# Performance work log

Hardware: AMD Instinct MI355X
Metric: run time of the kernel (lower is better)

## Reference

```python
import jax, jax.numpy as jnp
import numpy as np

NUM_GROUPS = 32
EPS = 1e-6


def group_norm(x, gamma, beta):
    # x: (B, C, H, W)
    B, C, H, W = x.shape
    g = x.reshape(B, NUM_GROUPS, C // NUM_GROUPS, H, W)
    mean = g.mean(axis=(2, 3, 4), keepdims=True)
    var = g.var(axis=(2, 3, 4), keepdims=True)
    g = (g - mean) / jnp.sqrt(var + EPS)
    g = g.reshape(B, C, H, W)
    return g * gamma[None, :, None, None] + beta[None, :, None, None]


def nin(x, W, b):
    # 1x1 linear projection over channel dim
    return jnp.einsum('bchw,cd->bdhw', x, W) + b[None, :, None, None]


def setup_inputs() -> dict:
    key = jax.random.key(0)
    ks = jax.random.split(key, 8)
    B, C, H, W = 32, 512, 32, 32
    lim = np.sqrt(3 * 0.1 / C)  # NIN init_scale=0.1 uniform limit
    return {
        'x': jax.random.normal(ks[0], (B, C, H, W), jnp.float32),
        'gamma': jnp.ones((C,), jnp.float32),
        'beta': jnp.zeros((C,), jnp.float32),
        'Wq': jax.random.uniform(ks[1], (C, C), jnp.float32, -lim, lim),
        'bq': jnp.zeros((C,), jnp.float32),
        'Wk': jax.random.uniform(ks[2], (C, C), jnp.float32, -lim, lim),
        'bk': jnp.zeros((C,), jnp.float32),
        'Wv': jax.random.uniform(ks[3], (C, C), jnp.float32, -lim, lim),
        'bv': jnp.zeros((C,), jnp.float32),
        'Wp': jax.random.normal(ks[4], (C, C), jnp.float32) * 1e-5,  # init_scale=0.0 -> ~0
        'bp': jnp.zeros((C,), jnp.float32),
    }


def reference(x, gamma, beta, Wq, bq, Wk, bk, Wv, bv, Wp, bp):
    B, C, H, W = x.shape
    h = group_norm(x, gamma, beta)
    q = nin(h, Wq, bq)
    k = nin(h, Wk, bk)
    v = nin(h, Wv, bv)
    # full (HW)x(HW) attention weights, as the original materializes
    w = jnp.einsum('bchw,bcHW->bhwHW', q, k) * (C ** -0.5)
    w = w.reshape(B, H, W, H * W)
    w = jax.nn.softmax(w, axis=-1)
    w = w.reshape(B, H, W, H, W)
    h_out = jnp.einsum('bhwHW,bcHW->bchw', w, v)
    h_out = nin(h_out, Wp, bp)
    return x + h_out
```

## Files before the change

### kernel.cpp

```cpp
#include <hip/hip_runtime.h>
#include <hip/hip_bf16.h>
#include <math.h>

typedef __attribute__((ext_vector_type(8))) short bf16x8;
typedef __attribute__((ext_vector_type(4))) float f32x4;

typedef const __attribute__((address_space(1))) unsigned int guint;
typedef __attribute__((address_space(3))) unsigned int luint;

static __device__ __forceinline__ short f2bf(float f) {
    union { float f; unsigned u; } a; a.f = f;
    unsigned r = 0x7FFFu + ((a.u >> 16) & 1u);
    return (short)((a.u + r) >> 16);
}
static __device__ __forceinline__ float bf2f(short s) {
    union { unsigned u; float f; } a;
    a.u = ((unsigned)(unsigned short)s) << 16;
    return a.f;
}

__global__ __launch_bounds__(256)
void prep_w(const float* __restrict__ Wq, const float* __restrict__ Wk,
            const float* __restrict__ Wp, const float* __restrict__ Wv,
            const float* __restrict__ bq, const float* __restrict__ bk,
            const float* __restrict__ bp, const float* __restrict__ bv,
            short* __restrict__ wT, float* __restrict__ bqk,
            float* __restrict__ b2, float qscale)
{
    const int z = blockIdx.z;
    const int t = threadIdx.x;
    if (z == 4) {
        if (blockIdx.y == 0 && blockIdx.x < 16) {
            __shared__ float red[256];
            const int o = blockIdx.x * 32 + (t >> 3);
            const int part = t & 7;
            float a = 0.f;
            for (int d = part * 64; d < part * 64 + 64; ++d)
                a += bv[d] * Wp[d * 512 + o];
            red[t] = a; __syncthreads();
            if (part < 4) red[t] += red[t + 4];
            __syncthreads();
            if (part < 2) red[t] += red[t + 2];
            __syncthreads();
            if (part == 0) b2[o] = red[t] + red[t + 1] + bp[o];
        } else if (blockIdx.y == 1 && blockIdx.x < 4) {
            int i = blockIdx.x * 256 + t;
            bqk[i] = (i < 512) ? bq[i] * qscale : bk[i - 512];
        }
        return;
    }
    const int tx = t & 31, ty = t >> 5;
    const int c0 = blockIdx.y * 32, d0 = blockIdx.x * 32;
    short* O = wT + (long long)z * 262144;
    if (z == 3) {
#pragma unroll
        for (int r = 0; r < 4; ++r) {
            const int idx = (c0 + ty + 8 * r) * 512 + d0 + tx;
            O[idx] = f2bf(Wv[idx]);
        }
        return;
    }
    __shared__ float ld[32][33];
    const float* W = (z == 0) ? Wq : (z == 1) ? Wk : Wp;
    const float sc = (z == 0) ? qscale : 1.f;
#pragma unroll
    for (int r = 0; r < 4; ++r)
        ld[ty + 8 * r][tx] = W[(long long)(c0 + ty + 8 * r) * 512 + d0 + tx];
    __syncthreads();
#pragma unroll
    for (int r = 0; r < 4; ++r)
        O[(long long)(d0 + ty + 8 * r) * 512 + c0 + tx] = f2bf(ld[tx][ty + 8 * r] * sc);
}

__global__ __launch_bounds__(256)
void small_nt(const short* __restrict__ A, const short* __restrict__ B,
              short* __restrict__ C, float scale, int K,
              int lda, int ldb, int ldc, int tilesM)
{
    __shared__ short lsA[128 * 64];
    __shared__ short lsB[128 * 64];
    const int m0 = (blockIdx.x % tilesM) * 128;
    const int n0 = (blockIdx.x / tilesM) * 128;
    const int t = threadIdx.x;
    const int lane = t & 63;
    const int w = t >> 6;
    const int wr = w >> 1, wc = w & 1;
    const int lr16 = lane & 15, lkg = lane >> 4;
    const int srow = 32 * w + (lane >> 3);
    const int scol = (lane & 7) * 8;
    const short* gA = A + (long long)(m0 + srow) * lda + scol;
    const short* gB = B + (long long)(n0 + srow) * ldb + scol;

    f32x4 acc[4][4];
#pragma unroll
    for (int i = 0; i < 4; ++i)
#pragma unroll
        for (int j = 0; j < 4; ++j) acc[i][j] = (f32x4){0.f, 0.f, 0.f, 0.f};

    const int nk = K >> 6;
    for (int kt = 0; kt < nk; ++kt) {
        const short* ga = gA + kt * 64;
        const short* gb = gB + kt * 64;
#pragma unroll
        for (int c = 0; c < 4; ++c) {
            __builtin_amdgcn_global_load_lds(
                (guint*)(ga + (long long)(8 * c) * lda),
                (luint*)&lsA[(32 * w + 8 * c) * 64], 16, 0, 0);
            __builtin_amdgcn_global_load_lds(
                (guint*)(gb + (long long)(8 * c) * ldb),
                (luint*)&lsB[(32 * w + 8 * c) * 64], 16, 0, 0);
        }
        __syncthreads();
#pragma unroll
        for (int ks = 0; ks < 2; ++ks) {
            bf16x8 af[4], bfr[4];
#pragma unroll
            for (int mi = 0; mi < 4; ++mi)
                af[mi] = *reinterpret_cast<const bf16x8*>(
                    &lsA[(wr * 64 + mi * 16 + lr16) * 64 + ks * 32 + lkg * 8]);
#pragma unroll
            for (int ni = 0; ni < 4; ++ni)
                bfr[ni] = *reinterpret_cast<const bf16x8*>(
                    &lsB[(wc * 64 + ni * 16 + lr16) * 64 + ks * 32 + lkg * 8]);
#pragma unroll
            for (int mi = 0; mi < 4; ++mi)
#pragma unroll
                for (int ni = 0; ni < 4; ++ni)
                    acc[mi][ni] = __builtin_amdgcn_mfma_f32_16x16x32_bf16(
                        af[mi], bfr[ni], acc[mi][ni], 0, 0, 0);
        }
        __syncthreads();
    }
#pragma unroll
    for (int mi = 0; mi < 4; ++mi)
#pragma unroll
        for (int ni = 0; ni < 4; ++ni) {
            const int col = n0 + wc * 64 + ni * 16 + lr16;
#pragma unroll
            for (int j = 0; j < 4; ++j) {
                const int rrow = m0 + wr * 64 + mi * 16 + lkg * 4 + j;
                C[(long long)rrow * ldc + col] = f2bf(acc[mi][ni][j] * scale);
            }
        }
}

__global__ __launch_bounds__(256)
void gn_fused(const float* __restrict__ x, const float* __restrict__ gamma,
              const float* __restrict__ beta, short* __restrict__ hn,
              short* __restrict__ hnT)
{
    __shared__ float xs[16 * 1024];
    __shared__ float red[256];
    const int bg = blockIdx.x;
    const int g  = bg & 31, b = bg >> 5;
    const int t  = threadIdx.x;
    const float4* px = reinterpret_cast<const float4*>(x + (long long)bg * 16384);
    float s = 0.f, ss = 0.f;
#pragma unroll
    for (int i = 0; i < 16; ++i) {
        float4 v = px[t + 256 * i];
        reinterpret_cast<float4*>(xs)[t + 256 * i] = v;
        s  += v.x + v.y + v.z + v.w;
        ss += v.x * v.x + v.y * v.y + v.z * v.z + v.w * v.w;
    }
    red[t] = s; __syncthreads();
    for (int o = 128; o > 0; o >>= 1) {
        if (t < o) red[t] += red[t + o];
        __syncthreads();
    }
    const float mean = red[0] * (1.f / 16384.f);
    __syncthreads();
    red[t] = ss; __syncthreads();
    for (int o = 128; o > 0; o >>= 1) {
        if (t < o) red[t] += red[t + o];
        __syncthreads();
    }
    const float var  = red[0] * (1.f / 16384.f) - mean * mean;
    const float rstd = rsqrtf(var + 1e-6f);

    const int half = t & 1;
    float ga[8], be[8];
#pragma unroll
    for (int cc = 0; cc < 8; ++cc) {
        ga[cc] = gamma[g * 16 + half * 8 + cc];
        be[cc] = beta[g * 16 + half * 8 + cc];
    }
    short* outB = hn + (long long)bg * 16384;
#pragma unroll
    for (int it = 0; it < 8; ++it) {
        const int sidx = it * 128 + (t >> 1);
        bf16x8 o;
#pragma unroll
        for (int cc = 0; cc < 8; ++cc) {
            float v = xs[(half * 8 + cc) * 1024 + sidx];
            o[cc] = f2bf((v - mean) * rstd * ga[cc] + be[cc]);
        }
        *reinterpret_cast<bf16x8*>(outB + sidx * 16 + half * 8) = o;
    }
    short* oT = hnT + ((long long)b * 512 + g * 16) * 1024;
#pragma unroll
    for (int cc = 0; cc < 16; ++cc) {
        const float g_ = gamma[g * 16 + cc], b_ = beta[g * 16 + cc];
        const int pos = t * 4;
        short4 o4;
        o4.x = f2bf((xs[cc * 1024 + pos + 0] - mean) * rstd * g_ + b_);
        o4.y = f2bf((xs[cc * 1024 + pos + 1] - mean) * rstd * g_ + b_);
        o4.z = f2bf((xs[cc * 1024 + pos + 2] - mean) * rstd * g_ + b_);
        o4.w = f2bf((xs[cc * 1024 + pos + 3] - mean) * rstd * g_ + b_);
        *reinterpret_cast<short4*>(oT + cc * 1024 + pos) = o4;
    }
}

template<int BIAS_M, int BIAS_N, int RESID, int EXPRS, int DIVROW4, int HN_A, int HN_B>
__global__ __launch_bounds__(512, 1)
void nt_gemm(const short* __restrict__ A, const short* __restrict__ B,
             void* __restrict__ Cv,
             const float* __restrict__ biasM, const float* __restrict__ biasN,
             const float* __restrict__ resid, float* __restrict__ rs,
             float scale, int K, int lda, int ldb, int ldc,
             long long sA, long long sB, long long sC,
             int tilesM, int tilesPerBatch)
{
    __shared__ short lsA[2][2][128 * 64];
    __shared__ short lsB[2][2][128 * 64];

    const int id = blockIdx.x;
    const int chunk = gridDim.x >> 3;
    const int gid = chunk ? ((id & 7) * chunk + (id >> 3)) : id;
    const int bz = gid / tilesPerBatch;
    const int tt = gid - bz * tilesPerBatch;
    const int m0 = (tt % tilesM) * 256;
    const int n0 = (tt / tilesM) * 256;

    const int t = threadIdx.x;
    const int lane = t & 63;
    const int w = t >> 6;
    const int wrs = w >> 1;
    const int wcs = w & 1;
    const int lr16 = lane & 15, lkg = lane >> 4;
    const int sw = lr16 & 7;

    const int srow = t >> 3;
    const int jch  = (t & 7) ^ (srow & 7);
    const int scol = jch * 8;

    const short* gA; int rsA, ktA;
    if (HN_A) {
        gA = A + ((long long)bz * 32 + (jch >> 1)) * 16384
               + (long long)(m0 + srow) * 16 + (jch & 1) * 8;
        rsA = 16; ktA = 65536;
    } else {
        gA = A + (long long)bz * sA + (long long)(m0 + srow) * lda + scol;
        rsA = lda; ktA = 64;
    }
    const short* gB; int rsB, ktB;
    if (HN_B) {
        gB = B + ((long long)bz * 32 + (jch >> 1)) * 16384
               + (long long)(n0 + srow) * 16 + (jch & 1) * 8;
        rsB = 16; ktB = 65536;
    } else {
        gB = B + (long long)bz * sB + (long long)(n0 + srow) * ldb + scol;
        rsB = ldb; ktB = 64;
    }

    f32x4 acc[4][2][4];
#pragma unroll
    for (int q = 0; q < 4; ++q)
#pragma unroll
        for (int i = 0; i < 2; ++i)
#pragma unroll
            for (int j = 0; j < 4; ++j) acc[q][i][j] = (f32x4){0.f, 0.f, 0.f, 0.f};

    const int nk = K >> 6;

#define STAGE_A(buf, h, kt)                                                    \
    {                                                                          \
        _Pragma("unroll")                                                      \
        for (int c = 0; c < 2; ++c)                                            \
            __builtin_amdgcn_global_load_lds(                                  \
                (guint*)(gA + (long long)(kt) * ktA                            \
                            + (long long)((h) * 128 + 64 * c) * rsA),          \
                (luint*)&lsA[buf][h][t * 8 + 4096 * c], 16, 0, 0);             \
    }
#define STAGE_B(buf, h, kt)                                                    \
    {                                                                          \
        _Pragma("unroll")                                                      \
        for (int c = 0; c < 2; ++c)                                            \
            __builtin_amdgcn_global_load_lds(                                  \
                (guint*)(gB + (long long)(kt) * ktB                            \
                            + (long long)((h) * 128 + 64 * c) * rsB),          \
                (luint*)&lsB[buf][h][t * 8 + 4096 * c], 16, 0, 0);             \
    }

#define LDA_HALF(dst, buf, h)                                                  \
    _Pragma("unroll")                                                          \
    for (int mi2 = 0; mi2 < 2; ++mi2)                                          \
        _Pragma("unroll")                                                      \
        for (int ks = 0; ks < 2; ++ks)                                         \
            dst[mi2][ks] = *reinterpret_cast<const bf16x8*>(                   \
                &lsA[buf][h][(wrs * 32 + mi2 * 16 + lr16) * 64 +               \
                             (((ks * 4 + lkg) ^ sw) * 8)]);
#define LDB_HALF(dst, buf, h)                                                  \
    _Pragma("unroll")                                                          \
    for (int ni = 0; ni < 4; ++ni)                                             \
        _Pragma("unroll")                                                      \
        for (int ks = 0; ks < 2; ++ks)                                         \
            dst[ni][ks] = *reinterpret_cast<const bf16x8*>(                    \
                &lsB[buf][h][(wcs * 64 + ni * 16 + lr16) * 64 +                \
                             (((ks * 4 + lkg) ^ sw) * 8)]);

#define MFMAQ(q, Af, Bf)                                                       \
    _Pragma("unroll")                                                          \
    for (int ks = 0; ks < 2; ++ks)                                             \
        _Pragma("unroll")                                                      \
        for (int mi2 = 0; mi2 < 2; ++mi2)                                      \
            _Pragma("unroll")                                                  \
            for (int ni = 0; ni < 4; ++ni)                                     \
                acc[q][mi2][ni] = __builtin_amdgcn_mfma_f32_16x16x32_bf16(     \
                    Af[mi2][ks], Bf[ni][ks], acc[q][mi2][ni], 0, 0, 0);

#define PH_END(N)                                                              \
    asm volatile("s_waitcnt vmcnt(" #N ")" ::: "memory");                      \
    __builtin_amdgcn_s_barrier();                                              \
    __builtin_amdgcn_sched_barrier(0)

#define FRAME(b, kt)                                                           \
    {                                                                          \
        bf16x8 a0[2][2], a1[2][2], b0f[4][2], b1f[4][2];                       \
           \
        LDB_HALF(b0f, b, 0)                                                    \
        LDA_HALF(a0, b, 0)                                                     \
        LDB_HALF(b1f, b, 1)                                                    \
        STAGE_B((b) ^ 1, 0, (kt) + 1);                                         \
        STAGE_B((b) ^ 1, 1, (kt) + 1);                                         \
        STAGE_A((b) ^ 1, 0, (kt) + 1);                                         \
        MFMAQ(0, a0, b0f)                                                      \
        MFMAQ(1, a0, b1f)                                                      \
        PH_END(6);                                                             \
              \
        LDA_HALF(a1, b, 1)                                                     \
        STAGE_A((b) ^ 1, 1, (kt) + 1);                                         \
        MFMAQ(2, a1, b0f)                                                      \
        MFMAQ(3, a1, b1f)                                                      \
        PH_END(2);                                                             \
    }

    STAGE_B(0, 0, 0); STAGE_B(0, 1, 0); STAGE_A(0, 0, 0);
    STAGE_A(0, 1, 0);
    PH_END(2);

    for (int kt = 0; kt < nk; kt += 2) {
        FRAME(0, kt)
        FRAME(1, kt + 1)
    }
#undef STAGE_A
#undef STAGE_B
#undef LDA_HALF
#undef LDB_HALF
#undef MFMAQ
#undef PH_END
#undef FRAME

    float psum[2][2][4];
    if (EXPRS) {
#pragma unroll
        for (int ah = 0; ah < 2; ++ah)
#pragma unroll
            for (int mi2 = 0; mi2 < 2; ++mi2)
#pragma unroll
                for (int j = 0; j < 4; ++j) psum[ah][mi2][j] = 0.f;
    }
#pragma unroll
    for (int ah = 0; ah < 2; ++ah) {
#pragma unroll
        for (int bh = 0; bh < 2; ++bh) {
#pragma unroll
            for (int mi2 = 0; mi2 < 2; ++mi2) {
                float addm[4], mul[4];
#pragma unroll
                for (int j = 0; j < 4; ++j) {
                    const int rrow = m0 + ah * 128 + wrs * 32 + mi2 * 16 + lkg * 4 + j;
                    addm[j] = BIAS_M ? biasM[rrow] : 0.f;
                    if (DIVROW4) {
                        const float* r4 = rs + (long long)bz * 4096 + rrow;
                        mul[j] = 1.f / (r4[0] + r4[1024] + r4[2048] + r4[3072]);
                    } else mul[j] = 1.f;
                }
#pragma unroll
                for (int ni = 0; ni < 4; ++ni) {
                    const int col = n0 + bh * 128 + wcs * 64 + ni * 16 + lr16;
                    float bn = BIAS_N ? biasN[col] : 0.f;
#pragma unroll
                    for (int j = 0; j < 4; ++j) {
                        const int rrow = m0 + ah * 128 + wrs * 32 + mi2 * 16 + lkg * 4 + j;
                        float v2 = acc[ah * 2 + bh][mi2][ni][j] + addm[j] + bn;
                        v2 *= scale;
                        if (EXPRS) { v2 = __expf(v2 - 8.f); psum[ah][mi2][j] += v2; }
                        if (DIVROW4) v2 *= mul[j];
                        const long long idx = (long long)rrow * ldc + col;
                        if (RESID) {
                            float* Cf = (float*)Cv + (long long)bz * sC;
                            Cf[idx] = v2 + resid[(long long)bz * sC + idx];
                        } else {
                            short* Cs = (short*)Cv + (long long)bz * sC;
                            Cs[idx] = f2bf(v2);
                        }
                    }
                }
            }
        }
    }
    if (EXPRS) {
#pragma unroll
        for (int ah = 0; ah < 2; ++ah)
#pragma unroll
            for (int mi2 = 0; mi2 < 2; ++mi2)
#pragma unroll
                for (int j = 0; j < 4; ++j) {
                    float v = psum[ah][mi2][j];
                    v += __shfl_xor(v, 1); v += __shfl_xor(v, 2);
                    v += __shfl_xor(v, 4); v += __shfl_xor(v, 8);
                    psum[ah][mi2][j] = v;
                }
        float* scr = (float*)&lsA[1][0][0];
        __syncthreads();
        if (lr16 == 0) {
#pragma unroll
            for (int ah = 0; ah < 2; ++ah)
#pragma unroll
                for (int mi2 = 0; mi2 < 2; ++mi2)
#pragma unroll
                    for (int j = 0; j < 4; ++j)
                        scr[wcs * 256 + ah * 128 + wrs * 32 + mi2 * 16 + lkg * 4 + j]
                            = psum[ah][mi2][j];
        }
        __syncthreads();
        if (t < 256)
            rs[(long long)bz * 4096 + (n0 >> 8) * 1024 + m0 + t]
                = scr[t] + scr[256 + t];
    }
}

extern "C" void kernel_launch(void* const* d_in, const int* in_sizes, int n_in,
                              void* d_out, int out_size, void* d_ws, size_t ws_size,
                              hipStream_t stream)
{
    (void)in_sizes; (void)n_in; (void)out_size; (void)ws_size;
    const float* x     = (const float*)d_in[0];
    const float* gamma = (const float*)d_in[1];
    const float* beta  = (const float*)d_in[2];
    const float* Wq = (const float*)d_in[3];
    const float* bq = (const float*)d_in[4];
    const float* Wk = (const float*)d_in[5];
    const float* bk = (const float*)d_in[6];
    const float* Wv = (const float*)d_in[7];
    const float* bv = (const float*)d_in[8];
    const float* Wp = (const float*)d_in[9];
    const float* bp = (const float*)d_in[10];
    float* out = (float*)d_out;

    char* ws = (char*)d_ws;
    short*  hnT  = (short*)ws;
    short*  qkb  = (short*)(ws + (32LL << 20));
    short*  hn   = (short*)(ws + (96LL << 20));
    short*  expS = (short*)(ws + (96LL << 20));
    short*  wT   = (short*)(ws + (160LL << 20));
    short*  Avp  = (short*)(ws + (162LL << 20));
    float*  bqk  = (float*)(ws + (162LL << 20) + (512 << 10));
    float*  b2   = bqk + 1024;
    short*  Phn  = qkb;
    float*  rs4  = (float*)d_out;

    const short* WqkT = wT;
    const short* WpT  = wT + 2 * 262144;
    const short* WvC  = wT + 3 * 262144;

    const float qscale = 0.044194173824159216f;

    prep_w<<<dim3(16, 16, 5), 256, 0, stream>>>(
        Wq, Wk, Wp, Wv, bq, bk, bp, bv, wT, bqk, b2, qscale);
    small_nt<<<16, 256, 0, stream>>>(WpT, WvC, Avp, 1.f, 512, 512, 512, 512, 4);

    gn_fused<<<dim3(1024), 256, 0, stream>>>(x, gamma, beta, hn, hnT);

    nt_gemm<0, 1, 0, 0, 0, 1, 0><<<512, 512, 0, stream>>>(
        hn, WqkT, qkb, nullptr, bqk, nullptr, nullptr, 1.f,
        512, 0, 512, 1024, 0, 0, 1024LL * 1024, 4, 16);
    nt_gemm<0, 0, 0, 1, 0, 0, 0><<<512, 512, 0, stream>>>(
        qkb, qkb + 512, expS, nullptr, nullptr, nullptr, rs4, 1.f,
        512, 1024, 1024, 1024, 1024LL * 1024, 1024LL * 1024, 1024LL * 1024, 4, 16);
    nt_gemm<0, 0, 0, 0, 1, 0, 0><<<256, 512, 0, stream>>>(
        expS, hnT, Phn, nullptr, nullptr, nullptr, rs4, 1.f,
        1024, 1024, 1024, 512, 1024LL * 1024, 512LL * 1024, 512LL * 1024, 4, 8);
    nt_gemm<1, 0, 1, 0, 0, 0, 0><<<256, 512, 0, stream>>>(
        Avp, Phn, out, b2, nullptr, x, nullptr, 1.f,
        512, 512, 512, 1024, 0, 512LL * 1024, 512LL * 1024, 2, 8);
}
```

Before: 198.9 us.

## Use 16-wave 1024-thread GEMM blocks with simple double-buffered K loop

The NT GEMM moves from 8 waves (each computing four 32x64 quadrants of a 256x256 tile) to 16 waves in a 4x4 grid, each owning a 64x64 subtile. The hand-split two-phase pipeline with partial vmcnt waits is replaced by one stage-next, compute-current frame per K step, with a full vmcnt(0) wait and barrier. This aims to raise the number of waves available to hide latency and to simplify scheduling, at the cost of a coarser sync that no longer overlaps global loads across phase boundaries. The row-sum reduction is widened to four column waves to match.

```diff
diff --git a/kernel.cpp b/kernel.cpp
--- a/kernel.cpp
+++ b/kernel.cpp
@@ -212,7 +212,7 @@
 }
 
 template<int BIAS_M, int BIAS_N, int RESID, int EXPRS, int DIVROW4, int HN_A, int HN_B>
-__global__ __launch_bounds__(512, 1)
+__global__ __launch_bounds__(1024, 1)
 void nt_gemm(const short* __restrict__ A, const short* __restrict__ B,
              void* __restrict__ Cv,
              const float* __restrict__ biasM, const float* __restrict__ biasN,
@@ -221,8 +221,8 @@
              long long sA, long long sB, long long sC,
              int tilesM, int tilesPerBatch)
 {
-    __shared__ short lsA[2][2][128 * 64];
-    __shared__ short lsB[2][2][128 * 64];
+    __shared__ short lsA[2][256 * 64];
+    __shared__ short lsB[2][256 * 64];
 
     const int id = blockIdx.x;
     const int chunk = gridDim.x >> 3;
@@ -235,8 +235,7 @@
     const int t = threadIdx.x;
     const int lane = t & 63;
     const int w = t >> 6;
-    const int wrs = w >> 1;
-    const int wcs = w & 1;
+    const int wm = w >> 2, wn = w & 3;
     const int lr16 = lane & 15, lkg = lane >> 4;
     const int sw = lr16 & 7;
 
@@ -244,7 +243,7 @@
     const int jch  = (t & 7) ^ (srow & 7);
     const int scol = jch * 8;
 
-    const short* gA; int rsA, ktA;
+    const short* gA; long long rsA; long long ktA;
     if (HN_A) {
         gA = A + ((long long)bz * 32 + (jch >> 1)) * 16384
                + (long long)(m0 + srow) * 16 + (jch & 1) * 8;
@@ -253,7 +252,7 @@
         gA = A + (long long)bz * sA + (long long)(m0 + srow) * lda + scol;
         rsA = lda; ktA = 64;
     }
-    const short* gB; int rsB, ktB;
+    const short* gB; long long rsB; long long ktB;
     if (HN_B) {
         gB = B + ((long long)bz * 32 + (jch >> 1)) * 16384
                + (long long)(n0 + srow) * 16 + (jch & 1) * 8;
@@ -263,181 +262,134 @@
         rsB = ldb; ktB = 64;
     }
 
-    f32x4 acc[4][2][4];
-#pragma unroll
-    for (int q = 0; q < 4; ++q)
-#pragma unroll
-        for (int i = 0; i < 2; ++i)
-#pragma unroll
-            for (int j = 0; j < 4; ++j) acc[q][i][j] = (f32x4){0.f, 0.f, 0.f, 0.f};
+    f32x4 acc[4][4];
+#pragma unroll
+    for (int i = 0; i < 4; ++i)
+#pragma unroll
+        for (int j = 0; j < 4; ++j) acc[i][j] = (f32x4){0.f, 0.f, 0.f, 0.f};
 
     const int nk = K >> 6;
 
-#define STAGE_A(buf, h, kt)                                                    \
+#define STAGE(buf, kt)                                                         \
     {                                                                          \
         _Pragma("unroll")                                                      \
-        for (int c = 0; c < 2; ++c)                                            \
+        for (int c = 0; c < 2; ++c) {                                          \
             __builtin_amdgcn_global_load_lds(                                  \
-                (guint*)(gA + (long long)(kt) * ktA                            \
-                            + (long long)((h) * 128 + 64 * c) * rsA),          \
-                (luint*)&lsA[buf][h][t * 8 + 4096 * c], 16, 0, 0);             \
-    }
-#define STAGE_B(buf, h, kt)                                                    \
+                (guint*)(gA + (long long)(kt) * ktA + (long long)(128 * c) * rsA), \
+                (luint*)&lsA[buf][t * 8 + 8192 * c], 16, 0, 0);                \
+            __builtin_amdgcn_global_load_lds(                                  \
+                (guint*)(gB + (long long)(kt) * ktB + (long long)(128 * c) * rsB), \
+                (luint*)&lsB[buf][t * 8 + 8192 * c], 16, 0, 0);                \
+        }                                                                      \
+    }
+
+#define TILE_END                                                               \
+    __builtin_amdgcn_sched_barrier(0);                                         \
+    asm volatile("s_waitcnt vmcnt(0)" ::: "memory");                           \
+    __builtin_amdgcn_s_barrier();                                              \
+    __builtin_amdgcn_sched_barrier(0)
+
+#define FRAME(b, kt)                                                           \
     {                                                                          \
+        STAGE((b) ^ 1, (kt) + 1);                                              \
+        bf16x8 af[4], bfr[4];                                                  \
         _Pragma("unroll")                                                      \
-        for (int c = 0; c < 2; ++c)                                            \
-            __builtin_amdgcn_global_load_lds(                                  \
-                (guint*)(gB + (long long)(kt) * ktB                            \
-                            + (long long)((h) * 128 + 64 * c) * rsB),          \
-                (luint*)&lsB[buf][h][t * 8 + 4096 * c], 16, 0, 0);             \
-    }
-
-#define LDA_HALF(dst, buf, h)                                                  \
-    _Pragma("unroll")                                                          \
-    for (int mi2 = 0; mi2 < 2; ++mi2)                                          \
-        _Pragma("unroll")                                                      \
-        for (int ks = 0; ks < 2; ++ks)                                         \
-            dst[mi2][ks] = *reinterpret_cast<const bf16x8*>(                   \
-                &lsA[buf][h][(wrs * 32 + mi2 * 16 + lr16) * 64 +               \
-                             (((ks * 4 + lkg) ^ sw) * 8)]);
-#define LDB_HALF(dst, buf, h)                                                  \
-    _Pragma("unroll")                                                          \
-    for (int ni = 0; ni < 4; ++ni)                                             \
-        _Pragma("unroll")                                                      \
-        for (int ks = 0; ks < 2; ++ks)                                         \
-            dst[ni][ks] = *reinterpret_cast<const bf16x8*>(                    \
-                &lsB[buf][h][(wcs * 64 + ni * 16 + lr16) * 64 +                \
-                             (((ks * 4 + lkg) ^ sw) * 8)]);
-
-#define MFMAQ(q, Af, Bf)                                                       \
-    _Pragma("unroll")                                                          \
-    for (int ks = 0; ks < 2; ++ks)                                             \
-        _Pragma("unroll")                                                      \
-        for (int mi2 = 0; mi2 < 2; ++mi2)                                      \
+        for (int ks = 0; ks < 2; ++ks) {                                       \
+            _Pragma("unroll")                                                  \
+            for (int mi = 0; mi < 4; ++mi)                                     \
+                af[mi] = *reinterpret_cast<const bf16x8*>(                     \
+                    &lsA[b][(wm * 64 + mi * 16 + lr16) * 64 +                  \
+                            (((ks * 4 + lkg) ^ sw) * 8)]);                     \
             _Pragma("unroll")                                                  \
             for (int ni = 0; ni < 4; ++ni)                                     \
-                acc[q][mi2][ni] = __builtin_amdgcn_mfma_f32_16x16x32_bf16(     \
-                    Af[mi2][ks], Bf[ni][ks], acc[q][mi2][ni], 0, 0, 0);
-
-#define PH_END(N)                                                              \
-    asm volatile("s_waitcnt vmcnt(" #N ")" ::: "memory");                      \
-    __builtin_amdgcn_s_barrier();                                              \
-    __builtin_amdgcn_sched_barrier(0)
-
-#define FRAME(b, kt)                                                           \
-    {                                                                          \
-        bf16x8 a0[2][2], a1[2][2], b0f[4][2], b1f[4][2];                       \
-           \
-        LDB_HALF(b0f, b, 0)                                                    \
-        LDA_HALF(a0, b, 0)                                                     \
-        LDB_HALF(b1f, b, 1)                                                    \
-        STAGE_B((b) ^ 1, 0, (kt) + 1);                                         \
-        STAGE_B((b) ^ 1, 1, (kt) + 1);                                         \
-        STAGE_A((b) ^ 1, 0, (kt) + 1);                                         \
-        MFMAQ(0, a0, b0f)                                                      \
-        MFMAQ(1, a0, b1f)                                                      \
-        PH_END(6);                                                             \
-              \
-        LDA_HALF(a1, b, 1)                                                     \
-        STAGE_A((b) ^ 1, 1, (kt) + 1);                                         \
-        MFMAQ(2, a1, b0f)                                                      \
-        MFMAQ(3, a1, b1f)                                                      \
-        PH_END(2);                                                             \
-    }
-
-    STAGE_B(0, 0, 0); STAGE_B(0, 1, 0); STAGE_A(0, 0, 0);
-    STAGE_A(0, 1, 0);
-    PH_END(2);
+                bfr[ni] = *reinterpret_cast<const bf16x8*>(                    \
+                    &lsB[b][(wn * 64 + ni * 16 + lr16) * 64 +                  \
+                            (((ks * 4 + lkg) ^ sw) * 8)]);                     \
+            _Pragma("unroll")                                                  \
+            for (int mi = 0; mi < 4; ++mi)                                     \
+                _Pragma("unroll")                                              \
+                for (int ni = 0; ni < 4; ++ni)                                 \
+                    acc[mi][ni] = __builtin_amdgcn_mfma_f32_16x16x32_bf16(     \
+                        af[mi], bfr[ni], acc[mi][ni], 0, 0, 0);                \
+        }                                                                      \
+        TILE_END;                                                              \
+    }
+
+    STAGE(0, 0);
+    TILE_END;
 
     for (int kt = 0; kt < nk; kt += 2) {
         FRAME(0, kt)
         FRAME(1, kt + 1)
     }
-#undef STAGE_A
-#undef STAGE_B
-#undef LDA_HALF
-#undef LDB_HALF
-#undef MFMAQ
-#undef PH_END
+#undef STAGE
+#undef TILE_END
 #undef FRAME
 
-    float psum[2][2][4];
+    float psum[4][4];
     if (EXPRS) {
 #pragma unroll
-        for (int ah = 0; ah < 2; ++ah)
-#pragma unroll
-            for (int mi2 = 0; mi2 < 2; ++mi2)
-#pragma unroll
-                for (int j = 0; j < 4; ++j) psum[ah][mi2][j] = 0.f;
-    }
-#pragma unroll
-    for (int ah = 0; ah < 2; ++ah) {
-#pragma unroll
-        for (int bh = 0; bh < 2; ++bh) {
-#pragma unroll
-            for (int mi2 = 0; mi2 < 2; ++mi2) {
-                float addm[4], mul[4];
-#pragma unroll
-                for (int j = 0; j < 4; ++j) {
-                    const int rrow = m0 + ah * 128 + wrs * 32 + mi2 * 16 + lkg * 4 + j;
-                    addm[j] = BIAS_M ? biasM[rrow] : 0.f;
-                    if (DIVROW4) {
-                        const float* r4 = rs + (long long)bz * 4096 + rrow;
-                        mul[j] = 1.f / (r4[0] + r4[1024] + r4[2048] + r4[3072]);
-                    } else mul[j] = 1.f;
-                }
-#pragma unroll
-                for (int ni = 0; ni < 4; ++ni) {
-                    const int col = n0 + bh * 128 + wcs * 64 + ni * 16 + lr16;
-                    float bn = BIAS_N ? biasN[col] : 0.f;
-#pragma unroll
-                    for (int j = 0; j < 4; ++j) {
-                        const int rrow = m0 + ah * 128 + wrs * 32 + mi2 * 16 + lkg * 4 + j;
-                        float v2 = acc[ah * 2 + bh][mi2][ni][j] + addm[j] + bn;
-                        v2 *= scale;
-                        if (EXPRS) { v2 = __expf(v2 - 8.f); psum[ah][mi2][j] += v2; }
-                        if (DIVROW4) v2 *= mul[j];
-                        const long long idx = (long long)rrow * ldc + col;
-                        if (RESID) {
-                            float* Cf = (float*)Cv + (long long)bz * sC;
-                            Cf[idx] = v2 + resid[(long long)bz * sC + idx];
-                        } else {
-                            short* Cs = (short*)Cv + (long long)bz * sC;
-                            Cs[idx] = f2bf(v2);
-                        }
-                    }
+        for (int mi = 0; mi < 4; ++mi)
+#pragma unroll
+            for (int j = 0; j < 4; ++j) psum[mi][j] = 0.f;
+    }
+#pragma unroll
+    for (int mi = 0; mi < 4; ++mi) {
+        float addm[4], mul[4];
+#pragma unroll
+        for (int j = 0; j < 4; ++j) {
+            const int rrow = m0 + wm * 64 + mi * 16 + lkg * 4 + j;
+            addm[j] = BIAS_M ? biasM[rrow] : 0.f;
+            if (DIVROW4) {
+                const float* r4 = rs + (long long)bz * 4096 + rrow;
+                mul[j] = 1.f / (r4[0] + r4[1024] + r4[2048] + r4[3072]);
+            } else mul[j] = 1.f;
+        }
+#pragma unroll
+        for (int ni = 0; ni < 4; ++ni) {
+            const int col = n0 + wn * 64 + ni * 16 + lr16;
+            float bn = BIAS_N ? biasN[col] : 0.f;
+#pragma unroll
+            for (int j = 0; j < 4; ++j) {
+                const int rrow = m0 + wm * 64 + mi * 16 + lkg * 4 + j;
+                float v2 = acc[mi][ni][j] + addm[j] + bn;
+                v2 *= scale;
+                if (EXPRS) { v2 = __expf(v2 - 8.f); psum[mi][j] += v2; }
+                if (DIVROW4) v2 *= mul[j];
+                const long long idx = (long long)rrow * ldc + col;
+                if (RESID) {
+                    float* Cf = (float*)Cv + (long long)bz * sC;
+                    Cf[idx] = v2 + resid[(long long)bz * sC + idx];
+                } else {
+                    short* Cs = (short*)Cv + (long long)bz * sC;
+                    Cs[idx] = f2bf(v2);
                 }
             }
         }
     }
     if (EXPRS) {
 #pragma unroll
-        for (int ah = 0; ah < 2; ++ah)
-#pragma unroll
-            for (int mi2 = 0; mi2 < 2; ++mi2)
-#pragma unroll
-                for (int j = 0; j < 4; ++j) {
-                    float v = psum[ah][mi2][j];
-                    v += __shfl_xor(v, 1); v += __shfl_xor(v, 2);
-                    v += __shfl_xor(v, 4); v += __shfl_xor(v, 8);
-                    psum[ah][mi2][j] = v;
-                }
-        float* scr = (float*)&lsA[1][0][0];
+        for (int mi = 0; mi < 4; ++mi)
+#pragma unroll
+            for (int j = 0; j < 4; ++j) {
+                float v = psum[mi][j];
+                v += __shfl_xor(v, 1); v += __shfl_xor(v, 2);
+                v += __shfl_xor(v, 4); v += __shfl_xor(v, 8);
+                psum[mi][j] = v;
+            }
+        float* scr = (float*)&lsA[0][0];
         __syncthreads();
         if (lr16 == 0) {
 #pragma unroll
-            for (int ah = 0; ah < 2; ++ah)
-#pragma unroll
-                for (int mi2 = 0; mi2 < 2; ++mi2)
-#pragma unroll
-                    for (int j = 0; j < 4; ++j)
-                        scr[wcs * 256 + ah * 128 + wrs * 32 + mi2 * 16 + lkg * 4 + j]
-                            = psum[ah][mi2][j];
+            for (int mi = 0; mi < 4; ++mi)
+#pragma unroll
+                for (int j = 0; j < 4; ++j)
+                    scr[wn * 256 + wm * 64 + mi * 16 + lkg * 4 + j] = psum[mi][j];
         }
         __syncthreads();
         if (t < 256)
             rs[(long long)bz * 4096 + (n0 >> 8) * 1024 + m0 + t]
-                = scr[t] + scr[256 + t];
+                = scr[t] + scr[256 + t] + scr[512 + t] + scr[768 + t];
     }
 }
 
@@ -483,16 +435,16 @@
 
     gn_fused<<<dim3(1024), 256, 0, stream>>>(x, gamma, beta, hn, hnT);
 
-    nt_gemm<0, 1, 0, 0, 0, 1, 0><<<512, 512, 0, stream>>>(
+    nt_gemm<0, 1, 0, 0, 0, 1, 0><<<512, 1024, 0, stream>>>(
         hn, WqkT, qkb, nullptr, bqk, nullptr, nullptr, 1.f,
         512, 0, 512, 1024, 0, 0, 1024LL * 1024, 4, 16);
-    nt_gemm<0, 0, 0, 1, 0, 0, 0><<<512, 512, 0, stream>>>(
+    nt_gemm<0, 0, 0, 1, 0, 0, 0><<<512, 1024, 0, stream>>>(
         qkb, qkb + 512, expS, nullptr, nullptr, nullptr, rs4, 1.f,
         512, 1024, 1024, 1024, 1024LL * 1024, 1024LL * 1024, 1024LL * 1024, 4, 16);
-    nt_gemm<0, 0, 0, 0, 1, 0, 0><<<256, 512, 0, stream>>>(
+    nt_gemm<0, 0, 0, 0, 1, 0, 0><<<256, 1024, 0, stream>>>(
         expS, hnT, Phn, nullptr, nullptr, nullptr, rs4, 1.f,
         1024, 1024, 1024, 512, 1024LL * 1024, 512LL * 1024, 512LL * 1024, 4, 8);
-    nt_gemm<1, 0, 1, 0, 0, 0, 0><<<256, 512, 0, stream>>>(
+    nt_gemm<1, 0, 1, 0, 0, 0, 0><<<256, 1024, 0, stream>>>(
         Avp, Phn, out, b2, nullptr, x, nullptr, 1.f,
         512, 512, 512, 1024, 0, 512LL * 1024, 512LL * 1024, 2, 8);
 }
```

Measured after the change: 212.3 us. 6.8% more time.
